# Optimization experiments

Measured on AMD Instinct MI355X. Metric: run time of the kernel, lower is better.

## Reference

```python
import jax, jax.numpy as jnp
import numpy as np

B, C, T, K = 64, 12, 2048, 2048
LMAX = 11            # max kernel length among {7,9,11}
CMAX = C - 1         # torch.randint(1, C) -> at most C-1 selected channels
PL = 1024            # left pad: covers max 'same' left pad = (dil*(len-1))//2 <= (T-1)//2
PR = 3412            # right pad: covers zero-weight padded taps (LMAX-1)*dil_max
A = 7.0              # softppv_param


def setup_inputs() -> dict:
    rng = np.random.default_rng(0)
    klens = rng.choice(np.array([7, 9, 11]), size=K)
    nch = rng.integers(1, C, size=K)  # 1..C-1 channels per kernel
    weights = np.zeros((K, CMAX, LMAX), np.float32)
    ch_idx = np.zeros((K, CMAX), np.int32)
    dils = np.zeros(K, np.int32)
    offs = np.zeros(K, np.int32)
    olens = np.zeros(K, np.int32)
    for k in range(K):
        n, L = int(nch[k]), int(klens[k])
        ch_idx[k, :n] = rng.permutation(C)[:n]
        w = rng.standard_normal((n, L)).astype(np.float32)
        w -= w.mean(axis=1, keepdims=True)  # per-channel mean-centering as in torch init
        weights[k, :n, :L] = w
        d = int(2.0 ** rng.uniform(0.0, np.log2((T - 1) / (L - 1))))
        dils[k] = d
        if rng.integers(0, 2) == 0:  # padding='same' (torch: left=total//2, right=rest)
            offs[k] = PL - (d * (L - 1)) // 2
            olens[k] = T
        else:                        # padding='valid'
            offs[k] = PL
            olens[k] = T - d * (L - 1)
    biases = rng.uniform(0.0, 1.0, size=K).astype(np.float32)
    x = jax.random.normal(jax.random.key(0), (B, C, T), jnp.float32)
    return {
        "x": x,
        "weights": jnp.asarray(weights),
        "biases": jnp.asarray(biases),
        "ch_idx": jnp.asarray(ch_idx),
        "dils": jnp.asarray(dils),
        "offs": jnp.asarray(offs),
        "olens": jnp.asarray(olens),
    }


def reference(x, weights, biases, ch_idx, dils, offs, olens):
    # x: (B, C, T). Zero-pad time axis once so every (same/valid, dilation) variant
    # becomes a pure gather with a per-kernel offset; zero-padded weight taps/channels
    # contribute nothing, so padded gathers are harmless.
    xpad = jnp.pad(x, ((0, 0), (0, 0), (PL, PR)))
    t = jnp.arange(T)
    l = jnp.arange(LMAX)

    def step(_, p):
        W, b, ch, d, off, olen = p
        pos = off + t[:, None] + l[None, :] * d            # (T, LMAX) tap positions
        Xg = xpad[:, ch, :][:, :, pos]                     # (B, CMAX, T, LMAX)
        y = jnp.einsum('bctl,cl->bt', Xg, W) + b           # cross-correlation + bias
        mask = t < olen                                    # valid output positions
        ppv = jnp.sum(jax.nn.sigmoid(A * y - 3.0) * mask, axis=-1) / olen
        mx = jnp.max(jnp.where(mask, y, -jnp.inf), axis=-1)
        return None, (ppv, mx)

    _, (ppvs, mxs) = jax.lax.scan(step, None, (weights, biases, ch_idx, dils, offs, olens))
    # torch concatenates [ppv_k, max_k] per kernel along the feature axis -> (B, 2K)
    return jnp.stack([ppvs.T, mxs.T], axis=-1).reshape(x.shape[0], 2 * K)
```

## Files before the change

kernel.cpp:

```cpp
#include <hip/hip_runtime.h>
#include <hip/hip_bf16.h>
#include <math.h>

#define B_SZ   64
#define C_SZ   12
#define T_SZ   2048
#define K_SZ   2048
#define LMAX   11
#define CMAX   11
#define PL_PAD 1024
#define A_PARAM 7.0f

#define NW     8
#define BLOCK_MAIN (NW * 64)
#define R      8

__global__ __launch_bounds__(256) void trb_kernel(const float* __restrict__ x,
                                                  __hip_bfloat16* __restrict__ xT) {
    const int c    = blockIdx.x;
    const int lane = threadIdx.x & 63;
    const int wid  = threadIdx.x >> 6;
    const int t0   = blockIdx.y * 128 + wid * 32;
    const float* xrow = x + ((size_t)lane * C_SZ + c) * T_SZ + t0;
    __hip_bfloat16* dst = xT + ((size_t)c * T_SZ + t0) * 64 + lane;
    #pragma unroll 8
    for (int i = 0; i < 32; ++i)
        dst[i * 64] = __float2bfloat16(xrow[i]);
}

__global__ __launch_bounds__(1024) void sched_kernel(const float* __restrict__ w,
                                                     unsigned* __restrict__ perm) {
    __shared__ unsigned key[K_SZ];
    const int tid = threadIdx.x;

    for (int k = tid; k < K_SZ; k += 1024) {
        const float* wk = w + (size_t)k * (CMAX * LMAX);
        int n = 0, L = 0;
        for (int e = 0; e < CMAX * LMAX; ++e) {
            if (wk[e] != 0.0f) {
                const int c = e / LMAX, l = e % LMAX;
                n = max(n, c + 1);
                L = max(L, l + 1);
            }
        }
        key[k] = ((unsigned)(n * L) << 11) | (unsigned)k;
    }
    __syncthreads();

    for (int ksz = 2; ksz <= K_SZ; ksz <<= 1) {
        for (int j = ksz >> 1; j > 0; j >>= 1) {
            for (int i = tid; i < K_SZ; i += 1024) {
                const int ixj = i ^ j;
                if (ixj > i) {
                    const unsigned a = key[i], b = key[ixj];
                    const bool sw = ((i & ksz) == 0) ? (a < b) : (a > b);
                    if (sw) { key[i] = b; key[ixj] = a; }
                }
            }
            __syncthreads();
        }
    }
    for (int i = tid; i < K_SZ; i += 1024)
        perm[i] = key[i] & 0x7FFu;
}

template<int LC>
__device__ __forceinline__ void conv_all(
    const __hip_bfloat16* __restrict__ xT,
    const int*   __restrict__ sCh,
    const float  (* __restrict__ sW)[LMAX],
    int n, int d, int offr, int olen, float bias,
    int lane, int wid, float& psum, float& pmax)
{
    constexpr int NV = R + LC - 1;
    const int nj   = (T_SZ + d - 1) / d;
    const int njb  = (nj + R - 1) / R;
    const int S    = (d >= NW) ? 1 : ((NW + d - 1) / d);
    const int len  = (njb + S - 1) / S;
    const int nunits = d * S;

    for (int u = wid; u < nunits; u += NW) {
        int q, seg;
        if (S == 1) { q = u; seg = 0; }
        else        { q = u % d; seg = u / d; }
        const int jb0 = seg * len;
        const int jb1 = min(njb, jb0 + len);

        for (int jb = jb0; jb < jb1; ++jb) {
            const int tq = q + jb * (R * d);
            if (tq >= T_SZ) break;
            const int tpos0 = tq + offr;

            float y[R];
            #pragma unroll
            for (int r = 0; r < R; ++r) y[r] = bias;

            const bool fast = (tpos0 >= 0) && (tpos0 + (NV - 1) * d < T_SZ);

            if (fast) {
                for (int c = 0; c < n; ++c) {
                    const int rb = __builtin_amdgcn_readfirstlane(sCh[c] * T_SZ + tpos0);
                    const __hip_bfloat16* rp = xT + ((size_t)rb << 6);
                    float v[NV];
                    #pragma unroll
                    for (int i = 0; i < NV; ++i) {
                        v[i] = __bfloat162float(rp[lane]);
                        rp += (d << 6);
                    }
                    #pragma unroll
                    for (int l = 0; l < LC; ++l) {
                        const float wl = sW[c][l];
                        #pragma unroll
                        for (int r = 0; r < R; ++r)
                            y[r] = fmaf(wl, v[l + r], y[r]);
                    }
                }
            } else {
                for (int c = 0; c < n; ++c) {
                    const int rb = __builtin_amdgcn_readfirstlane(sCh[c] * T_SZ);
                    const __hip_bfloat16* row = xT + ((size_t)rb << 6);
                    float v[NV];
                    #pragma unroll
                    for (int i = 0; i < NV; ++i) {
                        const int tp  = tpos0 + i * d;
                        const int tpc = min(max(tp, 0), T_SZ - 1);
                        const float f = __bfloat162float(row[(tpc << 6) + lane]);
                        v[i] = ((unsigned)tp < (unsigned)T_SZ) ? f : 0.0f;
                    }
                    #pragma unroll
                    for (int l = 0; l < LC; ++l) {
                        const float wl = sW[c][l];
                        #pragma unroll
                        for (int r = 0; r < R; ++r)
                            y[r] = fmaf(wl, v[l + r], y[r]);
                    }
                }
            }

            #pragma unroll
            for (int r = 0; r < R; ++r) {
                const int t = tq + r * d;
                if (t < olen) {
                    psum += 1.0f / (1.0f + __expf(3.0f - A_PARAM * y[r]));
                    pmax  = fmaxf(pmax, y[r]);
                }
            }
        }
    }
}

__global__ __launch_bounds__(BLOCK_MAIN, 8) void rocket_tr(
    const __hip_bfloat16* __restrict__ xT,
    const unsigned* __restrict__ perm,
    const float* __restrict__ weights,
    const float* __restrict__ biases,
    const int*   __restrict__ ch_idx,
    const int*   __restrict__ dils,
    const int*   __restrict__ offs,
    const int*   __restrict__ olens,
    float*       __restrict__ out)
{
    __shared__ float sW[CMAX][LMAX];
    __shared__ int   sCh[CMAX];
    __shared__ int   sMeta[2];
    __shared__ float sP[NW][64];
    __shared__ float sM[NW][64];

    const int k   = (int)perm[blockIdx.x];
    const int tid = threadIdx.x;

    if (tid < CMAX * LMAX)
        sW[tid / LMAX][tid % LMAX] = weights[(size_t)k * (CMAX * LMAX) + tid];
    if (tid < CMAX)
        sCh[tid] = ch_idx[(size_t)k * CMAX + tid];
    __syncthreads();

    if (tid == 0) {
        int n = 0, L = 0;
        for (int c = 0; c < CMAX; ++c) {
            bool nz = false;
            for (int l = 0; l < LMAX; ++l) {
                if (sW[c][l] != 0.0f) { nz = true; if (l + 1 > L) L = l + 1; }
            }
            if (nz) n = c + 1;
        }
        sMeta[0] = n; sMeta[1] = L;
    }
    __syncthreads();

    const int   n    = sMeta[0];
    const int   L    = sMeta[1];
    const int   d    = dils[k];
    const int   offr = offs[k] - PL_PAD;
    const int   olen = olens[k];
    const float bias = biases[k];
    const int   lane = tid & 63;
    const int   wid  = __builtin_amdgcn_readfirstlane(tid >> 6);

    float psum = 0.0f;
    float pmax = -INFINITY;

    if (L <= 7)
        conv_all<7 >(xT, sCh, sW, n, d, offr, olen, bias, lane, wid, psum, pmax);
    else if (L <= 9)
        conv_all<9 >(xT, sCh, sW, n, d, offr, olen, bias, lane, wid, psum, pmax);
    else
        conv_all<11>(xT, sCh, sW, n, d, offr, olen, bias, lane, wid, psum, pmax);

    sP[wid][lane] = psum;
    sM[wid][lane] = pmax;
    __syncthreads();

    if (tid < 64) {
        float s = 0.0f, m = -INFINITY;
        #pragma unroll
        for (int w = 0; w < NW; ++w) {
            s += sP[w][tid];
            m  = fmaxf(m, sM[w][tid]);
        }
        const float inv_olen = 1.0f / (float)olen;
        out[(size_t)tid * (2 * K_SZ) + 2 * k]     = s * inv_olen;
        out[(size_t)tid * (2 * K_SZ) + 2 * k + 1] = m;
    }
}

__global__ __launch_bounds__(256) void rocket_fallback(
    const float* __restrict__ x,
    const float* __restrict__ weights,
    const float* __restrict__ biases,
    const int*   __restrict__ ch_idx,
    const int*   __restrict__ dils,
    const int*   __restrict__ offs,
    const int*   __restrict__ olens,
    float*       __restrict__ out)
{
    __shared__ float sW[CMAX][LMAX];
    __shared__ int   sCh[CMAX];
    __shared__ float sRed[2][4];

    const int k   = blockIdx.x;
    const int tid = threadIdx.x;

    if (tid < CMAX * LMAX)
        sW[tid / LMAX][tid % LMAX] = weights[(size_t)k * (CMAX * LMAX) + tid];
    if (tid < CMAX)
        sCh[tid] = ch_idx[(size_t)k * CMAX + tid];
    __syncthreads();

    const int   d    = dils[k];
    const int   off  = offs[k] - PL_PAD;
    const int   olen = olens[k];
    const float bias = biases[k];
    const int   lane = tid & 63;
    const int   wid  = tid >> 6;

    for (int b = blockIdx.y; b < B_SZ; b += gridDim.y) {
        float psum = 0.0f, pmax = -INFINITY;
        for (int t = tid; t < T_SZ; t += 256) {
            float y = bias;
            for (int c = 0; c < CMAX; ++c) {
                const float* xb = x + ((size_t)b * C_SZ + sCh[c]) * T_SZ;
                int pos = off + t;
                for (int l = 0; l < LMAX; ++l) {
                    const float xv = ((unsigned)pos < (unsigned)T_SZ) ? xb[pos] : 0.0f;
                    y = fmaf(sW[c][l], xv, y);
                    pos += d;
                }
            }
            if (t < olen) {
                psum += 1.0f / (1.0f + __expf(3.0f - A_PARAM * y));
                pmax = fmaxf(pmax, y);
            }
        }
        for (int o = 32; o > 0; o >>= 1) {
            psum += __shfl_down(psum, o, 64);
            pmax  = fmaxf(pmax, __shfl_down(pmax, o, 64));
        }
        if (lane == 0) { sRed[0][wid] = psum; sRed[1][wid] = pmax; }
        __syncthreads();
        if (tid == 0) {
            const float s = sRed[0][0] + sRed[0][1] + sRed[0][2] + sRed[0][3];
            const float m = fmaxf(fmaxf(sRed[1][0], sRed[1][1]),
                                  fmaxf(sRed[1][2], sRed[1][3]));
            out[(size_t)b * (2 * K_SZ) + 2 * k]     = s / (float)olen;
            out[(size_t)b * (2 * K_SZ) + 2 * k + 1] = m;
        }
        __syncthreads();
    }
}

extern "C" void kernel_launch(void* const* d_in, const int* in_sizes, int n_in,
                              void* d_out, int out_size, void* d_ws, size_t ws_size,
                              hipStream_t stream) {
    const float* x       = (const float*)d_in[0];
    const float* weights = (const float*)d_in[1];
    const float* biases  = (const float*)d_in[2];
    const int*   ch_idx  = (const int*)  d_in[3];
    const int*   dils    = (const int*)  d_in[4];
    const int*   offs    = (const int*)  d_in[5];
    const int*   olens   = (const int*)  d_in[6];
    float*       out     = (float*)d_out;

    const size_t xt_bytes = (size_t)C_SZ * T_SZ * 64 * sizeof(__hip_bfloat16);
    const size_t need     = xt_bytes + K_SZ * sizeof(unsigned);

    if (ws_size >= need) {
        __hip_bfloat16* xT   = (__hip_bfloat16*)d_ws;
        unsigned*       perm = (unsigned*)((char*)d_ws + xt_bytes);
        dim3 tgrid(C_SZ, T_SZ / 128);
        trb_kernel<<<tgrid, 256, 0, stream>>>(x, xT);
        sched_kernel<<<1, 1024, 0, stream>>>(weights, perm);
        rocket_tr<<<K_SZ, BLOCK_MAIN, 0, stream>>>(xT, perm, weights, biases,
                                                   ch_idx, dils, offs, olens, out);
    } else {
        dim3 grid(K_SZ, 16);
        rocket_fallback<<<grid, 256, 0, stream>>>(x, weights, biases, ch_idx,
                                                  dils, offs, olens, out);
    }
}
```

Measured before the change: 749.8 us.

## Pair channels into packed FMA, skip masked outputs, rebalance work split

Processes two channels at once using packed f32x2 FMA (v_pk_fma_f32), pairing weights in shared memory and summing the two lanes at the end. Loops now stop at olen instead of T, skipping masked outputs for 'valid' kernels. The dilation-phase split now targets 64 work units instead of 8 for better load balance across waves, the schedule cost key now includes output length, and the occupancy hint drops from 8 to 6 to allow more registers. The trade-offs are extra loads for the padding channel when n is odd and higher register pressure.

```diff
diff --git a/kernel.cpp b/kernel.cpp
--- a/kernel.cpp
+++ b/kernel.cpp
@@ -8,12 +8,19 @@
 #define K_SZ   2048
 #define LMAX   11
 #define CMAX   11
+#define CP_MAX 6
 #define PL_PAD 1024
 #define A_PARAM 7.0f
 
 #define NW     8
 #define BLOCK_MAIN (NW * 64)
 #define R      8
+
+typedef float f32x2 __attribute__((ext_vector_type(2)));
+
+__device__ __forceinline__ f32x2 fma2(f32x2 a, f32x2 b, f32x2 c) {
+    return __builtin_elementwise_fma(a, b, c);
+}
 
 __global__ __launch_bounds__(256) void trb_kernel(const float* __restrict__ x,
                                                   __hip_bfloat16* __restrict__ xT) {
@@ -29,6 +36,7 @@
 }
 
 __global__ __launch_bounds__(1024) void sched_kernel(const float* __restrict__ w,
+                                                     const int* __restrict__ olens,
                                                      unsigned* __restrict__ perm) {
     __shared__ unsigned key[K_SZ];
     const int tid = threadIdx.x;
@@ -43,7 +51,8 @@
                 L = max(L, l + 1);
             }
         }
-        key[k] = ((unsigned)(n * L) << 11) | (unsigned)k;
+        const unsigned cost = (unsigned)(n * L) * (unsigned)((olens[k] + 255) >> 8);
+        key[k] = (cost << 11) | (unsigned)k;
     }
     __syncthreads();
 
@@ -68,14 +77,14 @@
 __device__ __forceinline__ void conv_all(
     const __hip_bfloat16* __restrict__ xT,
     const int*   __restrict__ sCh,
-    const float  (* __restrict__ sW)[LMAX],
-    int n, int d, int offr, int olen, float bias,
+    const f32x2  (* __restrict__ sWp)[CP_MAX],
+    int npair, int d, int offr, int olen, float bias,
     int lane, int wid, float& psum, float& pmax)
 {
     constexpr int NV = R + LC - 1;
-    const int nj   = (T_SZ + d - 1) / d;
+    const int nj   = (olen + d - 1) / d;
     const int njb  = (nj + R - 1) / R;
-    const int S    = (d >= NW) ? 1 : ((NW + d - 1) / d);
+    const int S    = (d >= 64) ? 1 : ((64 + d - 1) / d);
     const int len  = (njb + S - 1) / S;
     const int nunits = d * S;
 
@@ -88,51 +97,60 @@
 
         for (int jb = jb0; jb < jb1; ++jb) {
             const int tq = q + jb * (R * d);
-            if (tq >= T_SZ) break;
+            if (tq >= olen) break;
             const int tpos0 = tq + offr;
 
-            float y[R];
+            f32x2 y2[R];
             #pragma unroll
-            for (int r = 0; r < R; ++r) y[r] = bias;
+            for (int r = 0; r < R; ++r) y2[r] = f32x2{bias, 0.0f};
 
             const bool fast = (tpos0 >= 0) && (tpos0 + (NV - 1) * d < T_SZ);
 
             if (fast) {
-                for (int c = 0; c < n; ++c) {
-                    const int rb = __builtin_amdgcn_readfirstlane(sCh[c] * T_SZ + tpos0);
-                    const __hip_bfloat16* rp = xT + ((size_t)rb << 6);
-                    float v[NV];
+                for (int cp = 0; cp < npair; ++cp) {
+                    const int rbA = __builtin_amdgcn_readfirstlane(sCh[2*cp  ] * T_SZ + tpos0);
+                    const int rbB = __builtin_amdgcn_readfirstlane(sCh[2*cp+1] * T_SZ + tpos0);
+                    const __hip_bfloat16* rpA = xT + ((size_t)rbA << 6) + lane;
+                    const __hip_bfloat16* rpB = xT + ((size_t)rbB << 6) + lane;
+                    f32x2 v2[NV];
                     #pragma unroll
                     for (int i = 0; i < NV; ++i) {
-                        v[i] = __bfloat162float(rp[lane]);
-                        rp += (d << 6);
+                        v2[i].x = __bfloat162float(*rpA);
+                        v2[i].y = __bfloat162float(*rpB);
+                        rpA += (d << 6);
+                        rpB += (d << 6);
                     }
                     #pragma unroll
                     for (int l = 0; l < LC; ++l) {
-                        const float wl = sW[c][l];
+                        const f32x2 w2 = sWp[l][cp];
                         #pragma unroll
                         for (int r = 0; r < R; ++r)
-                            y[r] = fmaf(wl, v[l + r], y[r]);
+                            y2[r] = fma2(w2, v2[l + r], y2[r]);
                     }
                 }
             } else {
-                for (int c = 0; c < n; ++c) {
-                    const int rb = __builtin_amdgcn_readfirstlane(sCh[c] * T_SZ);
-                    const __hip_bfloat16* row = xT + ((size_t)rb << 6);
-                    float v[NV];
+                for (int cp = 0; cp < npair; ++cp) {
+                    const int rbA = __builtin_amdgcn_readfirstlane(sCh[2*cp  ] * T_SZ);
+                    const int rbB = __builtin_amdgcn_readfirstlane(sCh[2*cp+1] * T_SZ);
+                    const __hip_bfloat16* rowA = xT + ((size_t)rbA << 6) + lane;
+                    const __hip_bfloat16* rowB = xT + ((size_t)rbB << 6) + lane;
+                    f32x2 v2[NV];
                     #pragma unroll
                     for (int i = 0; i < NV; ++i) {
                         const int tp  = tpos0 + i * d;
                         const int tpc = min(max(tp, 0), T_SZ - 1);
-                        const float f = __bfloat162float(row[(tpc << 6) + lane]);
-                        v[i] = ((unsigned)tp < (unsigned)T_SZ) ? f : 0.0f;
+                        const bool ok = (unsigned)tp < (unsigned)T_SZ;
+                        const float a = __bfloat162float(rowA[(size_t)tpc << 6]);
+                        const float b = __bfloat162float(rowB[(size_t)tpc << 6]);
+                        v2[i].x = ok ? a : 0.0f;
+                        v2[i].y = ok ? b : 0.0f;
                     }
                     #pragma unroll
                     for (int l = 0; l < LC; ++l) {
-                        const float wl = sW[c][l];
+                        const f32x2 w2 = sWp[l][cp];
                         #pragma unroll
                         for (int r = 0; r < R; ++r)
-                            y[r] = fmaf(wl, v[l + r], y[r]);
+                            y2[r] = fma2(w2, v2[l + r], y2[r]);
                     }
                 }
             }
@@ -141,15 +159,16 @@
             for (int r = 0; r < R; ++r) {
                 const int t = tq + r * d;
                 if (t < olen) {
-                    psum += 1.0f / (1.0f + __expf(3.0f - A_PARAM * y[r]));
-                    pmax  = fmaxf(pmax, y[r]);
-                }
-            }
-        }
-    }
-}
-
-__global__ __launch_bounds__(BLOCK_MAIN, 8) void rocket_tr(
+                    const float y = y2[r].x + y2[r].y;
+                    psum += 1.0f / (1.0f + __expf(3.0f - A_PARAM * y));
+                    pmax  = fmaxf(pmax, y);
+                }
+            }
+        }
+    }
+}
+
+__global__ __launch_bounds__(BLOCK_MAIN, 6) void rocket_tr(
     const __hip_bfloat16* __restrict__ xT,
     const unsigned* __restrict__ perm,
     const float* __restrict__ weights,
@@ -161,7 +180,8 @@
     float*       __restrict__ out)
 {
     __shared__ float sW[CMAX][LMAX];
-    __shared__ int   sCh[CMAX];
+    __shared__ f32x2 sWp[LMAX][CP_MAX];
+    __shared__ int   sCh[2 * CP_MAX];
     __shared__ int   sMeta[2];
     __shared__ float sP[NW][64];
     __shared__ float sM[NW][64];
@@ -171,10 +191,17 @@
 
     if (tid < CMAX * LMAX)
         sW[tid / LMAX][tid % LMAX] = weights[(size_t)k * (CMAX * LMAX) + tid];
-    if (tid < CMAX)
-        sCh[tid] = ch_idx[(size_t)k * CMAX + tid];
-    __syncthreads();
-
+    if (tid < 2 * CP_MAX)
+        sCh[tid] = (tid < CMAX) ? ch_idx[(size_t)k * CMAX + tid] : 0;
+    __syncthreads();
+
+    if (tid < LMAX * CP_MAX) {
+        const int l  = tid / CP_MAX;
+        const int cp = tid % CP_MAX;
+        const float wa = sW[2 * cp][l];
+        const float wb = (2 * cp + 1 < CMAX) ? sW[2 * cp + 1][l] : 0.0f;
+        sWp[l][cp] = f32x2{wa, wb};
+    }
     if (tid == 0) {
         int n = 0, L = 0;
         for (int c = 0; c < CMAX; ++c) {
@@ -188,24 +215,25 @@
     }
     __syncthreads();
 
-    const int   n    = sMeta[0];
-    const int   L    = sMeta[1];
-    const int   d    = dils[k];
-    const int   offr = offs[k] - PL_PAD;
-    const int   olen = olens[k];
-    const float bias = biases[k];
-    const int   lane = tid & 63;
-    const int   wid  = __builtin_amdgcn_readfirstlane(tid >> 6);
+    const int   n     = sMeta[0];
+    const int   L     = sMeta[1];
+    const int   npair = (n + 1) >> 1;
+    const int   d     = dils[k];
+    const int   offr  = offs[k] - PL_PAD;
+    const int   olen  = olens[k];
+    const float bias  = biases[k];
+    const int   lane  = tid & 63;
+    const int   wid   = __builtin_amdgcn_readfirstlane(tid >> 6);
 
     float psum = 0.0f;
     float pmax = -INFINITY;
 
     if (L <= 7)
-        conv_all<7 >(xT, sCh, sW, n, d, offr, olen, bias, lane, wid, psum, pmax);
+        conv_all<7 >(xT, sCh, sWp, npair, d, offr, olen, bias, lane, wid, psum, pmax);
     else if (L <= 9)
-        conv_all<9 >(xT, sCh, sW, n, d, offr, olen, bias, lane, wid, psum, pmax);
+        conv_all<9 >(xT, sCh, sWp, npair, d, offr, olen, bias, lane, wid, psum, pmax);
     else
-        conv_all<11>(xT, sCh, sW, n, d, offr, olen, bias, lane, wid, psum, pmax);
+        conv_all<11>(xT, sCh, sWp, npair, d, offr, olen, bias, lane, wid, psum, pmax);
 
     sP[wid][lane] = psum;
     sM[wid][lane] = pmax;
@@ -309,7 +337,7 @@
         unsigned*       perm = (unsigned*)((char*)d_ws + xt_bytes);
         dim3 tgrid(C_SZ, T_SZ / 128);
         trb_kernel<<<tgrid, 256, 0, stream>>>(x, xT);
-        sched_kernel<<<1, 1024, 0, stream>>>(weights, perm);
+        sched_kernel<<<1, 1024, 0, stream>>>(weights, olens, perm);
         rocket_tr<<<K_SZ, BLOCK_MAIN, 0, stream>>>(xT, perm, weights, biases,
                                                    ch_idx, dils, offs, olens, out);
     } else {
```

New measurement: 882.5 us. +17.7%, slower.

## Switch to fp16 packed dot2 convolution and skip outputs beyond valid length

Applied to the files above, without the earlier changes.

The transposed input is stored as fp16 instead of bf16, and weights are packed into fp16 pairs. The inner convolution now uses v_dot2 (fdot2) on pairs of taps built with alignbit, which halves the FMA count. Work now stops at olen instead of T, so invalid tail outputs of 'valid' kernels are no longer computed. The schedule cost includes olen, and the wave-split threshold changes from NW to 64. fp16 storage of inputs and weights trades range for mantissa precision relative to bf16.

```diff
diff --git a/kernel.cpp b/kernel.cpp
--- a/kernel.cpp
+++ b/kernel.cpp
@@ -1,5 +1,4 @@
 #include <hip/hip_runtime.h>
-#include <hip/hip_bf16.h>
 #include <math.h>
 
 #define B_SZ   64
@@ -8,6 +7,7 @@
 #define K_SZ   2048
 #define LMAX   11
 #define CMAX   11
+#define MPMAX  6
 #define PL_PAD 1024
 #define A_PARAM 7.0f
 
@@ -15,20 +15,30 @@
 #define BLOCK_MAIN (NW * 64)
 #define R      8
 
-__global__ __launch_bounds__(256) void trb_kernel(const float* __restrict__ x,
-                                                  __hip_bfloat16* __restrict__ xT) {
+typedef _Float16 h2 __attribute__((ext_vector_type(2)));
+
+__device__ __forceinline__ h2 as_h2(unsigned u) {
+    union { unsigned u; h2 h; } cv; cv.u = u; return cv.h;
+}
+__device__ __forceinline__ unsigned as_u32(h2 h) {
+    union { h2 h; unsigned u; } cv; cv.h = h; return cv.u;
+}
+
+__global__ __launch_bounds__(256) void trh_kernel(const float* __restrict__ x,
+                                                  _Float16* __restrict__ xT) {
     const int c    = blockIdx.x;
     const int lane = threadIdx.x & 63;
     const int wid  = threadIdx.x >> 6;
     const int t0   = blockIdx.y * 128 + wid * 32;
     const float* xrow = x + ((size_t)lane * C_SZ + c) * T_SZ + t0;
-    __hip_bfloat16* dst = xT + ((size_t)c * T_SZ + t0) * 64 + lane;
+    _Float16* dst = xT + ((size_t)c * T_SZ + t0) * 64 + lane;
     #pragma unroll 8
     for (int i = 0; i < 32; ++i)
-        dst[i * 64] = __float2bfloat16(xrow[i]);
+        dst[i * 64] = (_Float16)xrow[i];
 }
 
 __global__ __launch_bounds__(1024) void sched_kernel(const float* __restrict__ w,
+                                                     const int* __restrict__ olens,
                                                      unsigned* __restrict__ perm) {
     __shared__ unsigned key[K_SZ];
     const int tid = threadIdx.x;
@@ -43,7 +53,8 @@
                 L = max(L, l + 1);
             }
         }
-        key[k] = ((unsigned)(n * L) << 11) | (unsigned)k;
+        const unsigned cost = (unsigned)(n * L) * (unsigned)((olens[k] + 127) >> 7);
+        key[k] = (cost << 11) | (unsigned)k;
     }
     __syncthreads();
 
@@ -66,16 +77,19 @@
 
 template<int LC>
 __device__ __forceinline__ void conv_all(
-    const __hip_bfloat16* __restrict__ xT,
-    const int*   __restrict__ sCh,
-    const float  (* __restrict__ sW)[LMAX],
+    const _Float16* __restrict__ xT,
+    const int*      __restrict__ sCh,
+    const unsigned  (* __restrict__ sWh)[MPMAX],
     int n, int d, int offr, int olen, float bias,
     int lane, int wid, float& psum, float& pmax)
 {
     constexpr int NV = R + LC - 1;
-    const int nj   = (T_SZ + d - 1) / d;
+    constexpr int MP = (LC + 1) / 2;
+    constexpr int PE = NV / 2;
+
+    const int nj   = (olen + d - 1) / d;
     const int njb  = (nj + R - 1) / R;
-    const int S    = (d >= NW) ? 1 : ((NW + d - 1) / d);
+    const int S    = (d >= 64) ? 1 : ((64 + d - 1) / d);
     const int len  = (njb + S - 1) / S;
     const int nunits = d * S;
 
@@ -88,7 +102,7 @@
 
         for (int jb = jb0; jb < jb1; ++jb) {
             const int tq = q + jb * (R * d);
-            if (tq >= T_SZ) break;
+            if (tq >= olen) break;
             const int tpos0 = tq + offr;
 
             float y[R];
@@ -100,39 +114,71 @@
             if (fast) {
                 for (int c = 0; c < n; ++c) {
                     const int rb = __builtin_amdgcn_readfirstlane(sCh[c] * T_SZ + tpos0);
-                    const __hip_bfloat16* rp = xT + ((size_t)rb << 6);
-                    float v[NV];
-                    #pragma unroll
-                    for (int i = 0; i < NV; ++i) {
-                        v[i] = __bfloat162float(rp[lane]);
-                        rp += (d << 6);
+                    const unsigned short* rp =
+                        (const unsigned short*)xT + ((size_t)rb << 6);
+                    unsigned wreg[MP];
+                    #pragma unroll
+                    for (int m = 0; m < MP; ++m) wreg[m] = sWh[c][m];
+
+                    unsigned pe[PE], po[PE];
+                    #pragma unroll
+                    for (int j = 0; j < PE; ++j) {
+                        const unsigned a = rp[lane]; rp += (d << 6);
+                        const unsigned b = rp[lane]; rp += (d << 6);
+                        pe[j] = a | (b << 16);
                     }
                     #pragma unroll
-                    for (int l = 0; l < LC; ++l) {
-                        const float wl = sW[c][l];
+                    for (int j = 0; j < PE - 1; ++j)
+                        po[j] = __builtin_amdgcn_alignbit(pe[j + 1], pe[j], 16);
+                    po[PE - 1] = pe[PE - 1] >> 16;
+
+                    #pragma unroll
+                    for (int m = 0; m < MP; ++m) {
+                        const h2 w2 = as_h2(wreg[m]);
                         #pragma unroll
-                        for (int r = 0; r < R; ++r)
-                            y[r] = fmaf(wl, v[l + r], y[r]);
+                        for (int r = 0; r < R; ++r) {
+                            const unsigned vp = (r & 1) ? po[m + ((r - 1) >> 1)]
+                                                        : pe[m + (r >> 1)];
+                            y[r] = __builtin_amdgcn_fdot2(w2, as_h2(vp), y[r], false);
+                        }
                     }
                 }
             } else {
                 for (int c = 0; c < n; ++c) {
                     const int rb = __builtin_amdgcn_readfirstlane(sCh[c] * T_SZ);
-                    const __hip_bfloat16* row = xT + ((size_t)rb << 6);
-                    float v[NV];
-                    #pragma unroll
-                    for (int i = 0; i < NV; ++i) {
-                        const int tp  = tpos0 + i * d;
-                        const int tpc = min(max(tp, 0), T_SZ - 1);
-                        const float f = __bfloat162float(row[(tpc << 6) + lane]);
-                        v[i] = ((unsigned)tp < (unsigned)T_SZ) ? f : 0.0f;
+                    const unsigned short* row =
+                        (const unsigned short*)xT + ((size_t)rb << 6);
+                    unsigned wreg[MP];
+                    #pragma unroll
+                    for (int m = 0; m < MP; ++m) wreg[m] = sWh[c][m];
+
+                    unsigned pe[PE], po[PE];
+                    #pragma unroll
+                    for (int j = 0; j < PE; ++j) {
+                        const int tp0 = tpos0 + (2 * j    ) * d;
+                        const int tp1 = tpos0 + (2 * j + 1) * d;
+                        const int c0  = min(max(tp0, 0), T_SZ - 1);
+                        const int c1  = min(max(tp1, 0), T_SZ - 1);
+                        unsigned a = row[((size_t)c0 << 6) + lane];
+                        unsigned b = row[((size_t)c1 << 6) + lane];
+                        a = ((unsigned)tp0 < (unsigned)T_SZ) ? a : 0u;
+                        b = ((unsigned)tp1 < (unsigned)T_SZ) ? b : 0u;
+                        pe[j] = a | (b << 16);
                     }
                     #pragma unroll
-                    for (int l = 0; l < LC; ++l) {
-                        const float wl = sW[c][l];
+                    for (int j = 0; j < PE - 1; ++j)
+                        po[j] = __builtin_amdgcn_alignbit(pe[j + 1], pe[j], 16);
+                    po[PE - 1] = pe[PE - 1] >> 16;
+
+                    #pragma unroll
+                    for (int m = 0; m < MP; ++m) {
+                        const h2 w2 = as_h2(wreg[m]);
                         #pragma unroll
-                        for (int r = 0; r < R; ++r)
-                            y[r] = fmaf(wl, v[l + r], y[r]);
+                        for (int r = 0; r < R; ++r) {
+                            const unsigned vp = (r & 1) ? po[m + ((r - 1) >> 1)]
+                                                        : pe[m + (r >> 1)];
+                            y[r] = __builtin_amdgcn_fdot2(w2, as_h2(vp), y[r], false);
+                        }
                     }
                 }
             }
@@ -150,7 +196,7 @@
 }
 
 __global__ __launch_bounds__(BLOCK_MAIN, 8) void rocket_tr(
-    const __hip_bfloat16* __restrict__ xT,
+    const _Float16* __restrict__ xT,
     const unsigned* __restrict__ perm,
     const float* __restrict__ weights,
     const float* __restrict__ biases,
@@ -160,11 +206,12 @@
     const int*   __restrict__ olens,
     float*       __restrict__ out)
 {
-    __shared__ float sW[CMAX][LMAX];
-    __shared__ int   sCh[CMAX];
-    __shared__ int   sMeta[2];
-    __shared__ float sP[NW][64];
-    __shared__ float sM[NW][64];
+    __shared__ float    sW[CMAX][LMAX];
+    __shared__ unsigned sWh[CMAX][MPMAX];
+    __shared__ int      sCh[CMAX];
+    __shared__ int      sMeta[2];
+    __shared__ float    sP[NW][64];
+    __shared__ float    sM[NW][64];
 
     const int k   = (int)perm[blockIdx.x];
     const int tid = threadIdx.x;
@@ -175,6 +222,14 @@
         sCh[tid] = ch_idx[(size_t)k * CMAX + tid];
     __syncthreads();
 
+    if (tid < CMAX * MPMAX) {
+        const int c = tid / MPMAX;
+        const int m = tid % MPMAX;
+        const float w0 = sW[c][2 * m];
+        const float w1 = (2 * m + 1 < LMAX) ? sW[c][2 * m + 1] : 0.0f;
+        h2 hh; hh.x = (_Float16)w0; hh.y = (_Float16)w1;
+        sWh[c][m] = as_u32(hh);
+    }
     if (tid == 0) {
         int n = 0, L = 0;
         for (int c = 0; c < CMAX; ++c) {
@@ -201,11 +256,11 @@
     float pmax = -INFINITY;
 
     if (L <= 7)
-        conv_all<7 >(xT, sCh, sW, n, d, offr, olen, bias, lane, wid, psum, pmax);
+        conv_all<7 >(xT, sCh, sWh, n, d, offr, olen, bias, lane, wid, psum, pmax);
     else if (L <= 9)
-        conv_all<9 >(xT, sCh, sW, n, d, offr, olen, bias, lane, wid, psum, pmax);
+        conv_all<9 >(xT, sCh, sWh, n, d, offr, olen, bias, lane, wid, psum, pmax);
     else
-        conv_all<11>(xT, sCh, sW, n, d, offr, olen, bias, lane, wid, psum, pmax);
+        conv_all<11>(xT, sCh, sWh, n, d, offr, olen, bias, lane, wid, psum, pmax);
 
     sP[wid][lane] = psum;
     sM[wid][lane] = pmax;
@@ -301,15 +356,15 @@
     const int*   olens   = (const int*)  d_in[6];
     float*       out     = (float*)d_out;
 
-    const size_t xt_bytes = (size_t)C_SZ * T_SZ * 64 * sizeof(__hip_bfloat16);
+    const size_t xt_bytes = (size_t)C_SZ * T_SZ * 64 * sizeof(_Float16);
     const size_t need     = xt_bytes + K_SZ * sizeof(unsigned);
 
     if (ws_size >= need) {
-        __hip_bfloat16* xT   = (__hip_bfloat16*)d_ws;
-        unsigned*       perm = (unsigned*)((char*)d_ws + xt_bytes);
+        _Float16* xT   = (_Float16*)d_ws;
+        unsigned* perm = (unsigned*)((char*)d_ws + xt_bytes);
         dim3 tgrid(C_SZ, T_SZ / 128);
-        trb_kernel<<<tgrid, 256, 0, stream>>>(x, xT);
-        sched_kernel<<<1, 1024, 0, stream>>>(weights, perm);
+        trh_kernel<<<tgrid, 256, 0, stream>>>(x, xT);
+        sched_kernel<<<1, 1024, 0, stream>>>(weights, olens, perm);
         rocket_tr<<<K_SZ, BLOCK_MAIN, 0, stream>>>(xT, perm, weights, biases,
                                                    ch_idx, dils, offs, olens, out);
     } else {
```

Result: slower. 809.0 us (+7.9%).

## Switch convolution to packed fp16 FMA with batch-pair layout and olen-aware scheduling

Applied to the files above, without the earlier changes.

The input is now transposed into packed half2 words that each hold two batch elements. Each lane splits its work by half-wave over time positions and runs packed fp16 FMAs, which doubles arithmetic throughput per instruction. Loops now stop at olen instead of T, and the scheduler's cost key includes olen, so valid-padding kernels do less work and are ordered better. The risk is fp16 accumulation precision: sums over up to 121 taps in half precision may exceed tolerance, and the half-wave time split makes the indexing and reduction more complex.

```diff
diff --git a/kernel.cpp b/kernel.cpp
--- a/kernel.cpp
+++ b/kernel.cpp
@@ -1,5 +1,4 @@
 #include <hip/hip_runtime.h>
-#include <hip/hip_bf16.h>
 #include <math.h>
 
 #define B_SZ   64
@@ -15,20 +14,22 @@
 #define BLOCK_MAIN (NW * 64)
 #define R      8
 
-__global__ __launch_bounds__(256) void trb_kernel(const float* __restrict__ x,
-                                                  __hip_bfloat16* __restrict__ xT) {
-    const int c    = blockIdx.x;
-    const int lane = threadIdx.x & 63;
-    const int wid  = threadIdx.x >> 6;
-    const int t0   = blockIdx.y * 128 + wid * 32;
-    const float* xrow = x + ((size_t)lane * C_SZ + c) * T_SZ + t0;
-    __hip_bfloat16* dst = xT + ((size_t)c * T_SZ + t0) * 64 + lane;
-    #pragma unroll 8
-    for (int i = 0; i < 32; ++i)
-        dst[i * 64] = __float2bfloat16(xrow[i]);
+typedef _Float16 h2 __attribute__((ext_vector_type(2)));
+
+__global__ __launch_bounds__(256) void trp_kernel(const float* __restrict__ x,
+                                                  unsigned* __restrict__ xT2) {
+    const int u  = blockIdx.x * 256 + threadIdx.x;
+    const int bp = u & 31;
+    const int t  = (u >> 5) & (T_SZ - 1);
+    const int c  = u >> 16;
+    const float a = x[((size_t)(2 * bp) * C_SZ + c) * T_SZ + t];
+    const float b = x[((size_t)(2 * bp + 1) * C_SZ + c) * T_SZ + t];
+    h2 v; v.x = (_Float16)a; v.y = (_Float16)b;
+    xT2[u] = __builtin_bit_cast(unsigned, v);
 }
 
 __global__ __launch_bounds__(1024) void sched_kernel(const float* __restrict__ w,
+                                                     const int* __restrict__ olens,
                                                      unsigned* __restrict__ perm) {
     __shared__ unsigned key[K_SZ];
     const int tid = threadIdx.x;
@@ -43,7 +44,8 @@
                 L = max(L, l + 1);
             }
         }
-        key[k] = ((unsigned)(n * L) << 11) | (unsigned)k;
+        const unsigned cost = (unsigned)(n * L) * (unsigned)((olens[k] + 127) >> 7);
+        key[k] = (cost << 11) | (unsigned)k;
     }
     __syncthreads();
 
@@ -66,18 +68,24 @@
 
 template<int LC>
 __device__ __forceinline__ void conv_all(
-    const __hip_bfloat16* __restrict__ xT,
-    const int*   __restrict__ sCh,
-    const float  (* __restrict__ sW)[LMAX],
-    int n, int d, int offr, int olen, float bias,
-    int lane, int wid, float& psum, float& pmax)
+    const unsigned* __restrict__ xT2,
+    const int*      __restrict__ sCh,
+    const unsigned  (* __restrict__ sWs)[LMAX],
+    int n, int d, int offr, int olen, unsigned bias2,
+    int bp, int h, int wid,
+    float& psum_lo, float& psum_hi, float& pmax_lo, float& pmax_hi)
 {
-    constexpr int NV = R + LC - 1;
-    const int nj   = (T_SZ + d - 1) / d;
-    const int njb  = (nj + R - 1) / R;
-    const int S    = (d >= NW) ? 1 : ((NW + d - 1) / d);
+    constexpr int NV   = R + LC - 1;
+    constexpr int SPAN = 2 * R + LC - 2;
+
+    const int nj   = (olen + d - 1) / d;
+    const int njb  = (nj + 2 * R - 1) / (2 * R);
+    const int S    = (d >= 64) ? 1 : ((64 + d - 1) / d);
     const int len  = (njb + S - 1) / S;
     const int nunits = d * S;
+
+    const int h8d   = h * (d << 3);
+    const int voffe = h * (d << 8) + bp;
 
     for (int u = wid; u < nunits; u += NW) {
         int q, seg;
@@ -87,62 +95,72 @@
         const int jb1 = min(njb, jb0 + len);
 
         for (int jb = jb0; jb < jb1; ++jb) {
-            const int tq = q + jb * (R * d);
-            if (tq >= T_SZ) break;
+            const int tq = q + jb * (2 * R * d);
+            if (tq >= olen) break;
             const int tpos0 = tq + offr;
 
-            float y[R];
+            h2 y2[R];
             #pragma unroll
-            for (int r = 0; r < R; ++r) y[r] = bias;
-
-            const bool fast = (tpos0 >= 0) && (tpos0 + (NV - 1) * d < T_SZ);
+            for (int r = 0; r < R; ++r) y2[r] = __builtin_bit_cast(h2, bias2);
+
+            const bool fast = (tpos0 >= 0) && (tpos0 + SPAN * d < T_SZ);
 
             if (fast) {
                 for (int c = 0; c < n; ++c) {
                     const int rb = __builtin_amdgcn_readfirstlane(sCh[c] * T_SZ + tpos0);
-                    const __hip_bfloat16* rp = xT + ((size_t)rb << 6);
-                    float v[NV];
+                    const unsigned* rp = xT2 + ((size_t)rb << 5);
+
+                    unsigned vp2[NV];
                     #pragma unroll
                     for (int i = 0; i < NV; ++i) {
-                        v[i] = __bfloat162float(rp[lane]);
-                        rp += (d << 6);
+                        vp2[i] = rp[voffe];
+                        rp += (d << 5);
                     }
+                    const unsigned* wrow = &sWs[c][0];
                     #pragma unroll
                     for (int l = 0; l < LC; ++l) {
-                        const float wl = sW[c][l];
+                        const h2 w = __builtin_bit_cast(h2, wrow[l]);
                         #pragma unroll
                         for (int r = 0; r < R; ++r)
-                            y[r] = fmaf(wl, v[l + r], y[r]);
+                            y2[r] = __builtin_elementwise_fma(
+                                w, __builtin_bit_cast(h2, vp2[l + r]), y2[r]);
                     }
                 }
             } else {
                 for (int c = 0; c < n; ++c) {
-                    const int rb = __builtin_amdgcn_readfirstlane(sCh[c] * T_SZ);
-                    const __hip_bfloat16* row = xT + ((size_t)rb << 6);
-                    float v[NV];
+                    const int rbs = __builtin_amdgcn_readfirstlane(sCh[c] * T_SZ);
+                    const unsigned* row = xT2 + ((size_t)rbs << 5);
+
+                    unsigned vp2[NV];
                     #pragma unroll
                     for (int i = 0; i < NV; ++i) {
-                        const int tp  = tpos0 + i * d;
+                        const int tp  = tpos0 + i * d + h8d;
                         const int tpc = min(max(tp, 0), T_SZ - 1);
-                        const float f = __bfloat162float(row[(tpc << 6) + lane]);
-                        v[i] = ((unsigned)tp < (unsigned)T_SZ) ? f : 0.0f;
+                        const unsigned v = row[(tpc << 5) + bp];
+                        vp2[i] = ((unsigned)tp < (unsigned)T_SZ) ? v : 0u;
                     }
+                    const unsigned* wrow = &sWs[c][0];
                     #pragma unroll
                     for (int l = 0; l < LC; ++l) {
-                        const float wl = sW[c][l];
+                        const h2 w = __builtin_bit_cast(h2, wrow[l]);
                         #pragma unroll
                         for (int r = 0; r < R; ++r)
-                            y[r] = fmaf(wl, v[l + r], y[r]);
+                            y2[r] = __builtin_elementwise_fma(
+                                w, __builtin_bit_cast(h2, vp2[l + r]), y2[r]);
                     }
                 }
             }
 
             #pragma unroll
             for (int r = 0; r < R; ++r) {
-                const int t = tq + r * d;
-                if (t < olen) {
-                    psum += 1.0f / (1.0f + __expf(3.0f - A_PARAM * y[r]));
-                    pmax  = fmaxf(pmax, y[r]);
+                const int tl = tq + r * d + h8d;
+                if (tl < olen) {
+                    const float ylo = (float)y2[r].x;
+                    const float yhi = (float)y2[r].y;
+                    psum_lo += 1.0f / (1.0f + __expf(3.0f - A_PARAM * ylo));
+                    psum_hi += 1.0f / (1.0f + __expf(3.0f - A_PARAM * yhi));
+                    pmax_lo  = fmaxf(pmax_lo, ylo);
+                    pmax_hi  = fmaxf(pmax_hi, yhi);
                 }
             }
         }
@@ -150,7 +168,7 @@
 }
 
 __global__ __launch_bounds__(BLOCK_MAIN, 8) void rocket_tr(
-    const __hip_bfloat16* __restrict__ xT,
+    const unsigned* __restrict__ xT2,
     const unsigned* __restrict__ perm,
     const float* __restrict__ weights,
     const float* __restrict__ biases,
@@ -160,11 +178,14 @@
     const int*   __restrict__ olens,
     float*       __restrict__ out)
 {
-    __shared__ float sW[CMAX][LMAX];
-    __shared__ int   sCh[CMAX];
-    __shared__ int   sMeta[2];
-    __shared__ float sP[NW][64];
-    __shared__ float sM[NW][64];
+    __shared__ float    sW[CMAX][LMAX];
+    __shared__ unsigned sWs[CMAX][LMAX];
+    __shared__ int      sCh[CMAX];
+    __shared__ int      sMeta[2];
+    __shared__ float    sPlo[NW][64];
+    __shared__ float    sPhi[NW][64];
+    __shared__ float    sMlo[NW][64];
+    __shared__ float    sMhi[NW][64];
 
     const int k   = (int)perm[blockIdx.x];
     const int tid = threadIdx.x;
@@ -175,6 +196,12 @@
         sCh[tid] = ch_idx[(size_t)k * CMAX + tid];
     __syncthreads();
 
+    if (tid < CMAX * LMAX) {
+        const int c = tid / LMAX, l = tid % LMAX;
+        const _Float16 wh = (_Float16)sW[c][l];
+        h2 hh; hh.x = wh; hh.y = wh;
+        sWs[c][l] = __builtin_bit_cast(unsigned, hh);
+    }
     if (tid == 0) {
         int n = 0, L = 0;
         for (int c = 0; c < CMAX; ++c) {
@@ -195,32 +222,50 @@
     const int   olen = olens[k];
     const float bias = biases[k];
     const int   lane = tid & 63;
+    const int   bp   = lane & 31;
+    const int   h    = lane >> 5;
     const int   wid  = __builtin_amdgcn_readfirstlane(tid >> 6);
 
-    float psum = 0.0f;
-    float pmax = -INFINITY;
+    const _Float16 bh = (_Float16)bias;
+    h2 bb; bb.x = bh; bb.y = bh;
+    const unsigned bias2 = __builtin_bit_cast(unsigned, bb);
+
+    float psum_lo = 0.0f, psum_hi = 0.0f;
+    float pmax_lo = -INFINITY, pmax_hi = -INFINITY;
 
     if (L <= 7)
-        conv_all<7 >(xT, sCh, sW, n, d, offr, olen, bias, lane, wid, psum, pmax);
+        conv_all<7 >(xT2, sCh, sWs, n, d, offr, olen, bias2, bp, h, wid,
+                     psum_lo, psum_hi, pmax_lo, pmax_hi);
     else if (L <= 9)
-        conv_all<9 >(xT, sCh, sW, n, d, offr, olen, bias, lane, wid, psum, pmax);
+        conv_all<9 >(xT2, sCh, sWs, n, d, offr, olen, bias2, bp, h, wid,
+                     psum_lo, psum_hi, pmax_lo, pmax_hi);
     else
-        conv_all<11>(xT, sCh, sW, n, d, offr, olen, bias, lane, wid, psum, pmax);
-
-    sP[wid][lane] = psum;
-    sM[wid][lane] = pmax;
+        conv_all<11>(xT2, sCh, sWs, n, d, offr, olen, bias2, bp, h, wid,
+                     psum_lo, psum_hi, pmax_lo, pmax_hi);
+
+    sPlo[wid][lane] = psum_lo;
+    sPhi[wid][lane] = psum_hi;
+    sMlo[wid][lane] = pmax_lo;
+    sMhi[wid][lane] = pmax_hi;
     __syncthreads();
 
     if (tid < 64) {
+        const int b   = tid;
+        const int bp2 = b >> 1;
+        const int odd = b & 1;
         float s = 0.0f, m = -INFINITY;
         #pragma unroll
         for (int w = 0; w < NW; ++w) {
-            s += sP[w][tid];
-            m  = fmaxf(m, sM[w][tid]);
+            const float s0 = odd ? sPhi[w][bp2]      : sPlo[w][bp2];
+            const float s1 = odd ? sPhi[w][32 + bp2] : sPlo[w][32 + bp2];
+            const float m0 = odd ? sMhi[w][bp2]      : sMlo[w][bp2];
+            const float m1 = odd ? sMhi[w][32 + bp2] : sMlo[w][32 + bp2];
+            s += s0 + s1;
+            m  = fmaxf(m, fmaxf(m0, m1));
         }
         const float inv_olen = 1.0f / (float)olen;
-        out[(size_t)tid * (2 * K_SZ) + 2 * k]     = s * inv_olen;
-        out[(size_t)tid * (2 * K_SZ) + 2 * k + 1] = m;
+        out[(size_t)b * (2 * K_SZ) + 2 * k]     = s * inv_olen;
+        out[(size_t)b * (2 * K_SZ) + 2 * k + 1] = m;
     }
 }
 
@@ -301,16 +346,16 @@
     const int*   olens   = (const int*)  d_in[6];
     float*       out     = (float*)d_out;
 
-    const size_t xt_bytes = (size_t)C_SZ * T_SZ * 64 * sizeof(__hip_bfloat16);
+    const size_t xt_bytes = (size_t)C_SZ * T_SZ * 32 * sizeof(unsigned);
     const size_t need     = xt_bytes + K_SZ * sizeof(unsigned);
 
     if (ws_size >= need) {
-        __hip_bfloat16* xT   = (__hip_bfloat16*)d_ws;
-        unsigned*       perm = (unsigned*)((char*)d_ws + xt_bytes);
-        dim3 tgrid(C_SZ, T_SZ / 128);
-        trb_kernel<<<tgrid, 256, 0, stream>>>(x, xT);
-        sched_kernel<<<1, 1024, 0, stream>>>(weights, perm);
-        rocket_tr<<<K_SZ, BLOCK_MAIN, 0, stream>>>(xT, perm, weights, biases,
+        unsigned* xT2  = (unsigned*)d_ws;
+        unsigned* perm = (unsigned*)((char*)d_ws + xt_bytes);
+        const int npk  = C_SZ * T_SZ * 32;
+        trp_kernel<<<npk / 256, 256, 0, stream>>>(x, xT2);
+        sched_kernel<<<1, 1024, 0, stream>>>(weights, olens, perm);
+        rocket_tr<<<K_SZ, BLOCK_MAIN, 0, stream>>>(xT2, perm, weights, biases,
                                                    ch_idx, dils, offs, olens, out);
     } else {
         dim3 grid(K_SZ, 16);
```

Result: slower. 1.022 ms (+36.3%).
